# Kernel optimization log

Hardware: AMD Instinct MI355X
Metric: run time of the kernel (lower is better)

Reference implementation:

```python
import jax, jax.numpy as jnp
import numpy as np
from jax import lax

B, T, HID, H, DK, DV, K = 2, 2048, 1024, 16, 64, 64, 4
SCALE = float(DK) ** -0.5
EPS = 1e-5


def setup_inputs() -> dict:
    key = jax.random.key(0)
    ks = jax.random.split(key, 12)
    n = lambda k, sh, s=0.02: (jax.random.normal(k, sh, jnp.float32) * s)
    return {
        "x": jax.random.normal(ks[0], (B, T, HID), jnp.float32),
        "Wq": n(ks[1], (H * DK, HID)),
        "Wk": n(ks[2], (H * DK, HID)),
        "Wv": n(ks[3], (H * DV, HID)),
        "Wa": n(ks[4], (H * DV, HID)), "ba": jnp.zeros((H * DV,), jnp.float32),
        "Wb": n(ks[5], (H, HID)), "bb": jnp.zeros((H,), jnp.float32),
        "Wg": n(ks[6], (H * DV, HID)),
        "Wo": n(ks[7], (HID, H * DV)),
        "qcw": n(ks[8], (H * DK, 1, K), 0.3), "qcb": jnp.zeros((H * DK,), jnp.float32),
        "kcw": n(ks[9], (H * DK, 1, K), 0.3), "kcb": jnp.zeros((H * DK,), jnp.float32),
        "vcw": n(ks[10], (H * DV, 1, K), 0.3), "vcb": jnp.zeros((H * DV,), jnp.float32),
        "ln_w": jnp.ones((DV,), jnp.float32), "ln_b": jnp.zeros((DV,), jnp.float32),
    }


def _causal_dwconv_silu(z, w, b):
    # z: [B,T,C], w: [C,1,K] depthwise. Conv1d(padding=K-1) then slice[:T] == causal left-pad.
    zc = z.transpose(0, 2, 1)  # [B,C,T]
    y = lax.conv_general_dilated(zc, w, (1,), [(K - 1, 0)],
                                 dimension_numbers=("NCH", "OIH", "NCH"),
                                 feature_group_count=zc.shape[1])
    return jax.nn.silu((y + b[None, :, None]).transpose(0, 2, 1))


def reference(x, Wq, Wk, Wv, Wa, ba, Wb, bb, Wg, Wo,
              qcw, qcb, kcw, kcb, vcw, vcb, ln_w, ln_b):
    Bb, Tt, _ = x.shape
    q = _causal_dwconv_silu(x @ Wq.T, qcw, qcb).reshape(Bb, Tt, H, DK)
    k = _causal_dwconv_silu(x @ Wk.T, kcw, kcb).reshape(Bb, Tt, H, DK) * SCALE
    v = _causal_dwconv_silu(x @ Wv.T, vcw, vcb).reshape(Bb, Tt, H, DV)
    a = jax.nn.sigmoid(x @ Wa.T + ba).reshape(Bb, Tt, H, DV)
    beta = jax.nn.sigmoid(x @ Wb.T + bb)  # [B,T,H]

    def step(S, inp):
        qt, kt, vt, at, bt = inp  # qt/kt: [B,H,DK], vt/at: [B,H,DV], bt: [B,H]
        err = jnp.einsum("bhij,bhj->bhi", S, kt) - vt          # S@k - v
        S = at[..., None] * S - bt[..., None, None] * (err[..., None] * kt[:, :, None, :])
        o = jnp.einsum("bhij,bhj->bhi", S, qt)                 # S@q
        return S, o

    xs = tuple(jnp.moveaxis(t, 1, 0) for t in (q, k, v, a, beta))  # time-leading
    S0 = jnp.zeros((Bb, H, DV, DK), x.dtype)
    _, o = lax.scan(step, S0, xs)
    o = jnp.moveaxis(o, 0, 1)  # [B,T,H,DV]

    mu = o.mean(-1, keepdims=True)
    var = ((o - mu) ** 2).mean(-1, keepdims=True)
    o = (o - mu) / jnp.sqrt(var + EPS) * ln_w + ln_b

    g = jax.nn.sigmoid(x @ Wg.T).reshape(Bb, Tt, H, DV)
    o = (o * g).reshape(Bb, Tt, H * DV)
    return o @ Wo.T
```

## Files before the change

kernel.cpp:

```cpp
#include <hip/hip_runtime.h>
#include <hip/hip_bf16.h>
#include <cstdint>


using bf16 = __hip_bfloat16;
typedef __bf16 bf16x8 __attribute__((ext_vector_type(8)));
typedef __bf16 bf16x4v __attribute__((ext_vector_type(4)));
typedef float f32x4 __attribute__((ext_vector_type(4)));
typedef float f32x2 __attribute__((ext_vector_type(2)));
typedef unsigned int u32x4 __attribute__((ext_vector_type(4)));
typedef unsigned int u32x2 __attribute__((ext_vector_type(2)));

__device__ __forceinline__ __bf16 cvt_bf16(float f) {
  __hip_bfloat16 h = (__hip_bfloat16)f;
  return *reinterpret_cast<__bf16*>(&h);
}
__device__ __forceinline__ void async_copy16(const void* g, void* l) {
  __builtin_amdgcn_global_load_lds((const __attribute__((address_space(1))) void*)g,
                                   (__attribute__((address_space(3))) void*)l,
                                   16, 0, 0);
}
__device__ __forceinline__ float bcf(unsigned int u) { return __builtin_bit_cast(float, u); }
template <int CTRL>
__device__ __forceinline__ float dpp_f(float x) {
  int y = __builtin_amdgcn_update_dpp(0, __builtin_bit_cast(int, x), CTRL, 0xF, 0xF, true);
  return __builtin_bit_cast(float, y);
}

__global__ __launch_bounds__(256) void cvtw_kernel(
    const float* __restrict__ x, const float* __restrict__ Wq,
    const float* __restrict__ Wk, const float* __restrict__ Wv,
    const float* __restrict__ Wa, const float* __restrict__ Wg,
    const float* __restrict__ Wo, bf16* __restrict__ xb,
    bf16* __restrict__ w4b, bf16* __restrict__ wgb, bf16* __restrict__ wob)
{
  int blk = blockIdx.x;
  const float* src;
  __bf16* dst;
  size_t off;
  if (blk < 4096) {
    src = x; dst = (__bf16*)xb;
    off = (size_t)blk * 1024 + threadIdx.x * 4;
  } else if (blk < 8192) {
    int wb = blk - 4096;
    int wi = wb >> 10;
    src = (wi == 0) ? Wq : (wi == 1) ? Wk : (wi == 2) ? Wv : Wa;
    dst = (__bf16*)w4b + (size_t)wi * 1024 * 1024;
    off = (size_t)(wb & 1023) * 1024 + threadIdx.x * 4;
  } else if (blk < 9216) {
    src = Wg; dst = (__bf16*)wgb;
    off = (size_t)(blk - 8192) * 1024 + threadIdx.x * 4;
  } else {
    src = Wo; dst = (__bf16*)wob;
    off = (size_t)(blk - 9216) * 1024 + threadIdx.x * 4;
  }
  float4 f = *(const float4*)(src + off);
  bf16x4v t;
  t[0] = cvt_bf16(f.x); t[1] = cvt_bf16(f.y); t[2] = cvt_bf16(f.z); t[3] = cvt_bf16(f.w);
  *(bf16x4v*)(dst + off) = t;
}

template <int MODE, bool A_FP32>
__global__ __launch_bounds__(256) void gemm_bt(
    const void* __restrict__ Av, const float* __restrict__ Bt,
    const float* __restrict__ bias, float* __restrict__ Cf, bf16* __restrict__ Cb,
    int M, int N, int K)
{
  __shared__ __align__(16) __bf16 As[128 * 32];
  __shared__ __align__(16) __bf16 Bs[128 * 32];

  const int tid  = threadIdx.x;
  const int lane = tid & 63;
  const int wave = tid >> 6;
  const int tile_m = blockIdx.y * 128;
  const int tile_n = blockIdx.x * 128;
  const int wm = (wave >> 1) * 64;
  const int wn = (wave & 1) * 64;

  const int srow = lane >> 2;
  const int scol = (lane & 3) * 8;

  f32x4 acc[4][4];
#pragma unroll
  for (int i = 0; i < 4; ++i)
#pragma unroll
    for (int j = 0; j < 4; ++j) acc[i][j] = {0.f, 0.f, 0.f, 0.f};

  for (int k0 = 0; k0 < K; k0 += 32) {
    float4 b0[2], b1[2], a0[2], a1[2];
#pragma unroll
    for (int s = 0; s < 2; ++s) {
      int brow = tile_n + s * 64 + wave * 16 + srow;
      if (brow > N - 1) brow = N - 1;
      const float* bp = Bt + (size_t)brow * K + k0 + scol;
      b0[s] = *(const float4*)bp;
      b1[s] = *(const float4*)(bp + 4);
      if (A_FP32) {
        int arow = tile_m + s * 64 + wave * 16 + srow;
        const float* ap = (const float*)Av + (size_t)arow * K + k0 + scol;
        a0[s] = *(const float4*)ap;
        a1[s] = *(const float4*)(ap + 4);
      }
    }
    __syncthreads();
#pragma unroll
    for (int s = 0; s < 2; ++s) {
      if (!A_FP32) {
        int arow = tile_m + s * 64 + wave * 16 + srow;
        async_copy16((const __bf16*)Av + (size_t)arow * K + k0 + scol,
                     &As[(s * 64 + wave * 16 + srow) * 32 + scol]);
      } else {
        bf16x8 ua;
        ua[0] = cvt_bf16(a0[s].x); ua[1] = cvt_bf16(a0[s].y);
        ua[2] = cvt_bf16(a0[s].z); ua[3] = cvt_bf16(a0[s].w);
        ua[4] = cvt_bf16(a1[s].x); ua[5] = cvt_bf16(a1[s].y);
        ua[6] = cvt_bf16(a1[s].z); ua[7] = cvt_bf16(a1[s].w);
        *(bf16x8*)&As[(s * 64 + wave * 16 + srow) * 32 + scol] = ua;
      }
      bf16x8 u;
      u[0] = cvt_bf16(b0[s].x); u[1] = cvt_bf16(b0[s].y);
      u[2] = cvt_bf16(b0[s].z); u[3] = cvt_bf16(b0[s].w);
      u[4] = cvt_bf16(b1[s].x); u[5] = cvt_bf16(b1[s].y);
      u[6] = cvt_bf16(b1[s].z); u[7] = cvt_bf16(b1[s].w);
      *(bf16x8*)&Bs[(s * 64 + wave * 16 + srow) * 32 + scol] = u;
    }
    __syncthreads();

    bf16x8 af[4], bfr[4];
#pragma unroll
    for (int i = 0; i < 4; ++i)
      af[i] = *(const bf16x8*)&As[(wm + i * 16 + (lane & 15)) * 32 + (lane >> 4) * 8];
#pragma unroll
    for (int j = 0; j < 4; ++j)
      bfr[j] = *(const bf16x8*)&Bs[(wn + j * 16 + (lane & 15)) * 32 + (lane >> 4) * 8];

#pragma unroll
    for (int i = 0; i < 4; ++i)
#pragma unroll
      for (int j = 0; j < 4; ++j)
        acc[i][j] = __builtin_amdgcn_mfma_f32_16x16x32_bf16(af[i], bfr[j], acc[i][j], 0, 0, 0);
  }

#pragma unroll
  for (int i = 0; i < 4; ++i) {
#pragma unroll
    for (int j = 0; j < 4; ++j) {
#pragma unroll
      for (int r = 0; r < 4; ++r) {
        int gm = tile_m + wm + i * 16 + (lane >> 4) * 4 + r;
        int gn = tile_n + wn + j * 16 + (lane & 15);
        if (gn < N) {
          float val = acc[i][j][r];
          if (MODE == 3 || MODE == 5) {
            float bv = bias ? bias[gn] : 0.f;
            val = 1.f / (1.f + __expf(-(val + bv)));
          }
          if (MODE == 4)      Cf[(size_t)gm * N + gn] = val;
          else if (MODE == 5) Cf[(size_t)gn * M + gm] = val;
          else                Cb[(size_t)gm * N + gn] = (bf16)val;
        }
      }
    }
  }
}

__global__ __launch_bounds__(256) void gemm_bb_ln(
    const bf16* __restrict__ o, const bf16* __restrict__ g,
    const float* __restrict__ lnw, const float* __restrict__ lnb,
    const bf16* __restrict__ Bw, float* __restrict__ C)
{
  __shared__ __align__(16) __bf16 As2[64][72];
  __shared__ __align__(16) __bf16 Bs2[2][128][32];
  __shared__ float sW[64], sB[64];

  const int bx = blockIdx.x;
  const int logical = (bx & 7) * 64 + (bx >> 3);
  const int tile_m = (logical >> 3) * 64;
  const int tile_n = (logical & 7) * 128;

  const int tid  = threadIdx.x;
  const int lane = tid & 63;
  const int wave = tid >> 6;
  const int wm = (wave >> 1) * 32;
  const int wn = (wave & 1) * 64;
  const int srow = lane >> 2;
  const int scol = (lane & 3) * 8;
  const int rl  = tid >> 2;
  const int qtr = tid & 3;

  if (tid < 64) { sW[tid] = lnw[tid]; sB[tid] = lnb[tid]; }

  const __bf16* obase = (const __bf16*)o + (size_t)(tile_m + rl) * 1024 + qtr * 16;
  const __bf16* gbase = (const __bf16*)g + (size_t)(tile_m + rl) * 1024 + qtr * 16;

  f32x4 acc[2][4];
#pragma unroll
  for (int i = 0; i < 2; ++i)
#pragma unroll
    for (int j = 0; j < 4; ++j) acc[i][j] = {0.f, 0.f, 0.f, 0.f};

  bf16x8 ov0, ov1, gv0, gv1;
  ov0 = *(const bf16x8*)(obase);
  ov1 = *(const bf16x8*)(obase + 8);
  gv0 = *(const bf16x8*)(gbase);
  gv1 = *(const bf16x8*)(gbase + 8);

  for (int h = 0; h < 16; ++h) {
    bf16x8 no0, no1, ng0, ng1;
    if (h + 1 < 16) {
      const __bf16* op = obase + (h + 1) * 64;
      const __bf16* gp = gbase + (h + 1) * 64;
      no0 = *(const bf16x8*)(op);
      no1 = *(const bf16x8*)(op + 8);
      ng0 = *(const bf16x8*)(gp);
      ng1 = *(const bf16x8*)(gp + 8);
    }

    __syncthreads();

#pragma unroll
    for (int sub = 0; sub < 2; ++sub)
#pragma unroll
      for (int s = 0; s < 2; ++s) {
        int brow = tile_n + s * 64 + wave * 16 + srow;
        async_copy16((const __bf16*)Bw + (size_t)brow * 1024 + h * 64 + sub * 32 + scol,
                     &Bs2[sub][s * 64 + wave * 16 + srow][scol]);
      }

    float sum = 0.f;
#pragma unroll
    for (int e = 0; e < 8; ++e)
      sum += (float)ov0[e] + (float)ov1[e];
    sum += __shfl_xor(sum, 1);
    sum += __shfl_xor(sum, 2);
    float mu = sum * (1.f / 64.f);
    float vv = 0.f;
#pragma unroll
    for (int e = 0; e < 8; ++e) {
      float d0 = (float)ov0[e] - mu, d1 = (float)ov1[e] - mu;
      vv += d0 * d0 + d1 * d1;
    }
    vv += __shfl_xor(vv, 1);
    vv += __shfl_xor(vv, 2);
    float rstd = rsqrtf(vv * (1.f / 64.f) + 1e-5f);

    bf16x8 res0, res1;
#pragma unroll
    for (int e = 0; e < 8; ++e) {
      int c0 = qtr * 16 + e;
      res0[e] = cvt_bf16((((float)ov0[e] - mu) * rstd * sW[c0] + sB[c0]) * (float)gv0[e]);
      res1[e] = cvt_bf16((((float)ov1[e] - mu) * rstd * sW[c0 + 8] + sB[c0 + 8]) * (float)gv1[e]);
    }
    *(bf16x8*)&As2[rl][qtr * 16 + 0] = res0;
    *(bf16x8*)&As2[rl][qtr * 16 + 8] = res1;

    __syncthreads();

#pragma unroll
    for (int sub = 0; sub < 2; ++sub) {
      bf16x8 af[2], bfr[4];
#pragma unroll
      for (int i = 0; i < 2; ++i)
        af[i] = *(const bf16x8*)&As2[wm + i * 16 + (lane & 15)][(lane >> 4) * 8 + sub * 32];
#pragma unroll
      for (int j = 0; j < 4; ++j)
        bfr[j] = *(const bf16x8*)&Bs2[sub][wn + j * 16 + (lane & 15)][(lane >> 4) * 8];

#pragma unroll
      for (int i = 0; i < 2; ++i)
#pragma unroll
        for (int j = 0; j < 4; ++j)
          acc[i][j] = __builtin_amdgcn_mfma_f32_16x16x32_bf16(af[i], bfr[j], acc[i][j], 0, 0, 0);
    }

    if (h + 1 < 16) {
      ov0 = no0; ov1 = no1;
      gv0 = ng0; gv1 = ng1;
    }
  }

#pragma unroll
  for (int i = 0; i < 2; ++i)
#pragma unroll
    for (int j = 0; j < 4; ++j)
#pragma unroll
      for (int r = 0; r < 4; ++r) {
        int gm = tile_m + wm + i * 16 + (lane >> 4) * 4 + r;
        int gn = tile_n + wn + j * 16 + (lane & 15);
        C[(size_t)gm * 1024 + gn] = acc[i][j][r];
      }
}

__global__ __launch_bounds__(256) void mega_gemm2(
    const bf16* __restrict__ Av, const bf16* __restrict__ W4b,
    const float* __restrict__ Wb, const float* __restrict__ bb,
    const float* __restrict__ ba, bf16* __restrict__ C4,
    float* __restrict__ betab)
{
  __shared__ __align__(16) __bf16 As[128 * 32];
  __shared__ __align__(16) __bf16 Bs[128 * 32];

  const int bx = blockIdx.x;
  const bool isbeta = (bx >= 1024);
  int tile_m, tile_n;
  if (!isbeta) {
    const int xcd = bx & 7;
    const int local = bx >> 3;
    const int mg = xcd >> 1;
    const int ng = xcd & 1;
    const int lm = local & 7;
    const int ln = local >> 3;
    tile_m = (mg * 8 + lm) * 128;
    tile_n = (ng * 16 + ln) * 128;
  } else {
    tile_m = (bx - 1024) * 128;
    tile_n = 0;
  }
  const int grp = tile_n >> 10;
  const int tnl = tile_n & 1023;

  const int tid  = threadIdx.x;
  const int lane = tid & 63;
  const int wave = tid >> 6;
  const int wm = (wave >> 1) * 64;
  const int wn = (wave & 1) * 64;

  const int srow = lane >> 2;
  const int scol = (lane & 3) * 8;

  f32x4 acc[4][4];
#pragma unroll
  for (int i = 0; i < 4; ++i)
#pragma unroll
    for (int j = 0; j < 4; ++j) acc[i][j] = {0.f, 0.f, 0.f, 0.f};

  const __bf16* Wp = (const __bf16*)W4b + (size_t)grp * 1024 * 1024;

  for (int k0 = 0; k0 < 1024; k0 += 32) {
    float4 b0[2], b1[2];
    if (isbeta) {
#pragma unroll
      for (int s = 0; s < 2; ++s) {
        int brow = s * 64 + wave * 16 + srow;
        if (brow > 15) brow = 15;
        const float* bp = Wb + (size_t)brow * 1024 + k0 + scol;
        b0[s] = *(const float4*)bp;
        b1[s] = *(const float4*)(bp + 4);
      }
    }
    __syncthreads();
#pragma unroll
    for (int s = 0; s < 2; ++s) {
      int arow = tile_m + s * 64 + wave * 16 + srow;
      async_copy16((const __bf16*)Av + (size_t)arow * 1024 + k0 + scol,
                   &As[(s * 64 + wave * 16 + srow) * 32 + scol]);
      if (!isbeta) {
        int brow = tnl + s * 64 + wave * 16 + srow;
        async_copy16(Wp + (size_t)brow * 1024 + k0 + scol,
                     &Bs[(s * 64 + wave * 16 + srow) * 32 + scol]);
      } else {
        bf16x8 u;
        u[0] = cvt_bf16(b0[s].x); u[1] = cvt_bf16(b0[s].y);
        u[2] = cvt_bf16(b0[s].z); u[3] = cvt_bf16(b0[s].w);
        u[4] = cvt_bf16(b1[s].x); u[5] = cvt_bf16(b1[s].y);
        u[6] = cvt_bf16(b1[s].z); u[7] = cvt_bf16(b1[s].w);
        *(bf16x8*)&Bs[(s * 64 + wave * 16 + srow) * 32 + scol] = u;
      }
    }
    __syncthreads();

    bf16x8 af[4], bfr[4];
#pragma unroll
    for (int i = 0; i < 4; ++i)
      af[i] = *(const bf16x8*)&As[(wm + i * 16 + (lane & 15)) * 32 + (lane >> 4) * 8];
#pragma unroll
    for (int j = 0; j < 4; ++j)
      bfr[j] = *(const bf16x8*)&Bs[(wn + j * 16 + (lane & 15)) * 32 + (lane >> 4) * 8];

#pragma unroll
    for (int i = 0; i < 4; ++i)
#pragma unroll
      for (int j = 0; j < 4; ++j)
        acc[i][j] = __builtin_amdgcn_mfma_f32_16x16x32_bf16(af[i], bfr[j], acc[i][j], 0, 0, 0);
  }

  if (!isbeta) {
    bf16* Cp = (bf16*)((__bf16*)C4 + (size_t)grp * 4096 * 1024);
#pragma unroll
    for (int i = 0; i < 4; ++i)
#pragma unroll
      for (int j = 0; j < 4; ++j)
#pragma unroll
        for (int r = 0; r < 4; ++r) {
          int gm = tile_m + wm + i * 16 + (lane >> 4) * 4 + r;
          int col = tnl + wn + j * 16 + (lane & 15);
          float val = acc[i][j][r];
          if (grp == 3) val = 1.f / (1.f + __expf(-(val + ba[col])));
          ((__bf16*)Cp)[(size_t)gm * 1024 + col] = cvt_bf16(val);
        }
  } else {
#pragma unroll
    for (int i = 0; i < 4; ++i)
#pragma unroll
      for (int j = 0; j < 4; ++j)
#pragma unroll
        for (int r = 0; r < 4; ++r) {
          int gm = tile_m + wm + i * 16 + (lane >> 4) * 4 + r;
          int gn = wn + j * 16 + (lane & 15);
          if (gn < 16) {
            float val = 1.f / (1.f + __expf(-(acc[i][j][r] + bb[gn])));
            betab[(size_t)gn * 4096 + gm] = val;
          }
        }
  }
}

__device__ __forceinline__ void conv_body(
    int idx, const bf16* __restrict__ z, const float* __restrict__ w,
    const float* __restrict__ bias, bf16* __restrict__ out, float scale)
{
  int c8 = idx & 127;
  int m  = idx >> 7;
  int t  = m & 2047;
  int c0 = c8 * 8;

  const __bf16* base = (const __bf16*)z + (size_t)m * 1024 + c0;
  const bf16x8 zzero = __builtin_bit_cast(bf16x8, (u32x4){0u, 0u, 0u, 0u});
  bf16x8 z3 = *(const bf16x8*)base;
  bf16x8 z2 = (t >= 1) ? *(const bf16x8*)(base - 1024) : zzero;
  bf16x8 z1 = (t >= 2) ? *(const bf16x8*)(base - 2048) : zzero;
  bf16x8 z0 = (t >= 3) ? *(const bf16x8*)(base - 3072) : zzero;

  const float* wp = w + c0 * 4;
  bf16x8 res;
#pragma unroll
  for (int e = 0; e < 8; ++e) {
    float4 we = *(const float4*)(wp + e * 4);
    float acc = bias[c0 + e] + (float)z3[e] * we.w;
    acc += (float)z2[e] * we.z;
    acc += (float)z1[e] * we.y;
    acc += (float)z0[e] * we.x;
    float s = acc / (1.f + __expf(-acc));
    res[e] = cvt_bf16(s * scale);
  }
  *(bf16x8*)((__bf16*)out + (size_t)m * 1024 + c0) = res;
}

__global__ __launch_bounds__(256) void conv_silu_kernel(
    const bf16* __restrict__ z, const float* __restrict__ w,
    const float* __restrict__ bias, bf16* __restrict__ out, float scale)
{
  conv_body(blockIdx.x * 256 + threadIdx.x, z, w, bias, out, scale);
}

__global__ __launch_bounds__(256) void conv2_kernel(
    const bf16* __restrict__ zq, const bf16* __restrict__ zk,
    const float* __restrict__ qcw, const float* __restrict__ qcb,
    const float* __restrict__ kcw, const float* __restrict__ kcb,
    bf16* __restrict__ oq, bf16* __restrict__ ok)
{
  int sec = blockIdx.x >> 11;
  int bx  = blockIdx.x & 2047;
  int idx = bx * 256 + threadIdx.x;
  if (sec == 0) conv_body(idx, zq, qcw, qcb, oq, 1.f);
  else          conv_body(idx, zk, kcw, kcb, ok, 0.125f);
}

__global__ __launch_bounds__(256) void convv_kk_kernel(
    const bf16* __restrict__ zv, const float* __restrict__ vcw,
    const float* __restrict__ vcb, bf16* __restrict__ ov,
    const bf16* __restrict__ k, const float* __restrict__ betab,
    float* __restrict__ G)
{
  if (blockIdx.x < 2048) {
    conv_body(blockIdx.x * 256 + threadIdx.x, zv, vcw, vcb, ov, 1.f);
    return;
  }
  int gtid = (blockIdx.x - 2048) * 256 + threadIdx.x;
  int out = gtid >> 2;
  int j   = gtid & 3;
  int h = out >> 12;
  int m = out & 4095;
  int t = m & 2047;
  float s = 0.f;
  if (t > 0) {
    const __bf16* r1 = (const __bf16*)k + (size_t)m * 1024 + h * 64 + j * 16;
    const __bf16* r0 = r1 - 1024;
    bf16x8 a0 = *(const bf16x8*)r0;
    bf16x8 a1 = *(const bf16x8*)(r0 + 8);
    bf16x8 b0 = *(const bf16x8*)r1;
    bf16x8 b1 = *(const bf16x8*)(r1 + 8);
#pragma unroll
    for (int e = 0; e < 8; ++e)
      s += (float)a0[e] * (float)b0[e] + (float)a1[e] * (float)b1[e];
  }
  s += __shfl_xor(s, 1);
  s += __shfl_xor(s, 2);
  if (j == 0) G[out] = betab[out] * s;
}

__global__ __launch_bounds__(256) void kk_kernel(
    const bf16* __restrict__ k, const float* __restrict__ betab,
    float* __restrict__ G)
{
  int tid = blockIdx.x * 256 + threadIdx.x;
  int out = tid >> 2;
  int j   = tid & 3;
  int h = out >> 12;
  int m = out & 4095;
  int t = m & 2047;
  float s = 0.f;
  if (t > 0) {
    const __bf16* r1 = (const __bf16*)k + (size_t)m * 1024 + h * 64 + j * 16;
    const __bf16* r0 = r1 - 1024;
    bf16x8 a0 = *(const bf16x8*)r0;
    bf16x8 a1 = *(const bf16x8*)(r0 + 8);
    bf16x8 b0 = *(const bf16x8*)r1;
    bf16x8 b1 = *(const bf16x8*)(r1 + 8);
#pragma unroll
    for (int e = 0; e < 8; ++e)
      s += (float)a0[e] * (float)b0[e] + (float)a1[e] * (float)b1[e];
  }
  s += __shfl_xor(s, 1);
  s += __shfl_xor(s, 2);
  if (j == 0) G[out] = betab[out] * s;
}

#define SCAN_STEP(i, KN0, KN1, Q0, Q1, WV, WA, BT, GT, LAST)                  \
  {                                                                           \
    const float vr = ((i) & 1) ? bcf((WV) & 0xffff0000u) : bcf((WV) << 16);   \
    const float ar = ((i) & 1) ? bcf((WA) & 0xffff0000u) : bcf((WA) << 16);   \
    float unxt = 0.f;                                                         \
    f32x2 k2n0 = {0.f, 0.f}, k2n1 = {0.f, 0.f};                               \
    if (!(LAST)) {                                                            \
      k2n0 = unpk(KN0); k2n1 = unpk(KN1);                                     \
      f32x2 dd = S20 * k2n0; dd += S21 * k2n1;                                \
      unxt = dd[0] + dd[1];                                                   \
      unxt += dpp_f<0xB1>(unxt);  unxt += dpp_f<0x4E>(unxt);                  \
      unxt += dpp_f<0x141>(unxt); unxt += dpp_f<0x140>(unxt);                 \
    } else { Sold0 = S20; Sold1 = S21; }                                      \
    float A_ = (BT) * __builtin_fmaf(aprev, u, -vr);                          \
    cc = __builtin_fmaf(-cc, (GT), A_);                                       \
    f32x2 q20 = unpk(Q0), q21 = unpk(Q1);                                     \
    const f32x2 cc2 = {cc, cc}, arv = {ar, ar};                               \
    f32x2 oo;                                                                 \
    { f32x2 t0 = cc2 * k2c0; S20 = arv * S20 - t0; oo = S20 * q20;            \
      f32x2 t1 = cc2 * k2c1; S21 = arv * S21 - t1; oo += S21 * q21; }         \
    so[(i)][lane] = oo[0] + oo[1];                                            \
    aprev = ar;                                                               \
    if (!(LAST)) { k2c0 = k2n0; k2c1 = k2n1; u = unxt; }                      \
  }

#define LOADG(KS, QS, VS, AS, BS, GS, g)                                      \
  KS = *(const u32x4*)&skT[buf][sg][(g) * 8];                                 \
  QS = *(const u32x4*)&sqT[buf][sg][(g) * 8];                                 \
  VS = *(const unsigned int*)&svaT[buf][0][r4][(g) * 2];                      \
  AS = *(const unsigned int*)&svaT[buf][1][r4][(g) * 2];                      \
  BS = *(const f32x2*)&sbeta[c * 16 + (g) * 2];                               \
  GS = *(const f32x2*)&sG[c * 16 + (g) * 2];

__global__ __launch_bounds__(256) void scan_gemm_kernel(
    const bf16* __restrict__ q, const bf16* __restrict__ k,
    const bf16* __restrict__ v, const bf16* __restrict__ a,
    const float* __restrict__ betab, const float* __restrict__ gkk,
    bf16* __restrict__ o,
    const float* __restrict__ x, const bf16* __restrict__ Wgb,
    bf16* __restrict__ gout)
{
  __shared__ __align__(16) __bf16 skT[2][16][72];
  __shared__ __align__(16) __bf16 sqT[2][16][72];
  __shared__ __align__(16) __bf16 svaT[2][2][4][16];
  __shared__ __align__(16) float  so[16][68];
  __shared__ __align__(16) __bf16 so2[16][4];
  __shared__ float sbeta[2048];
  __shared__ float sG[2048];
  __shared__ __align__(16) __bf16 As[128 * 32];
  __shared__ __align__(16) __bf16 Bs[128 * 32];

  if (blockIdx.x >= 512) {
    const int gb   = blockIdx.x - 512;
    const int tid  = threadIdx.x;
    const int lane = tid & 63;
    const int wave = tid >> 6;
    const int tile_m = (gb >> 3) * 128;
    const int tile_n = (gb & 7) * 128;
    const int wm = (wave >> 1) * 64;
    const int wn = (wave & 1) * 64;
    const int srow = lane >> 2;
    const int scol = (lane & 3) * 8;

    f32x4 acc[4][4];
#pragma unroll
    for (int i = 0; i < 4; ++i)
#pragma unroll
      for (int j = 0; j < 4; ++j) acc[i][j] = {0.f, 0.f, 0.f, 0.f};

    for (int k0 = 0; k0 < 1024; k0 += 32) {
      float4 a0[2], a1[2];
#pragma unroll
      for (int s = 0; s < 2; ++s) {
        int arow = tile_m + s * 64 + wave * 16 + srow;
        const float* ap = x + (size_t)arow * 1024 + k0 + scol;
        a0[s] = *(const float4*)ap;
        a1[s] = *(const float4*)(ap + 4);
      }
      __syncthreads();
#pragma unroll
      for (int s = 0; s < 2; ++s) {
        bf16x8 ua;
        ua[0] = cvt_bf16(a0[s].x); ua[1] = cvt_bf16(a0[s].y);
        ua[2] = cvt_bf16(a0[s].z); ua[3] = cvt_bf16(a0[s].w);
        ua[4] = cvt_bf16(a1[s].x); ua[5] = cvt_bf16(a1[s].y);
        ua[6] = cvt_bf16(a1[s].z); ua[7] = cvt_bf16(a1[s].w);
        *(bf16x8*)&As[(s * 64 + wave * 16 + srow) * 32 + scol] = ua;
        int brow = tile_n + s * 64 + wave * 16 + srow;
        async_copy16((const __bf16*)Wgb + (size_t)brow * 1024 + k0 + scol,
                     &Bs[(s * 64 + wave * 16 + srow) * 32 + scol]);
      }
      __syncthreads();

      bf16x8 af[4], bfr[4];
#pragma unroll
      for (int i = 0; i < 4; ++i)
        af[i] = *(const bf16x8*)&As[(wm + i * 16 + (lane & 15)) * 32 + (lane >> 4) * 8];
#pragma unroll
      for (int j = 0; j < 4; ++j)
        bfr[j] = *(const bf16x8*)&Bs[(wn + j * 16 + (lane & 15)) * 32 + (lane >> 4) * 8];

#pragma unroll
      for (int i = 0; i < 4; ++i)
#pragma unroll
        for (int j = 0; j < 4; ++j)
          acc[i][j] = __builtin_amdgcn_mfma_f32_16x16x32_bf16(af[i], bfr[j], acc[i][j], 0, 0, 0);
    }

#pragma unroll
    for (int i = 0; i < 4; ++i)
#pragma unroll
      for (int j = 0; j < 4; ++j)
#pragma unroll
        for (int r = 0; r < 4; ++r) {
          int gm = tile_m + wm + i * 16 + (lane >> 4) * 4 + r;
          int gn = tile_n + wn + j * 16 + (lane & 15);
          float val = 1.f / (1.f + __expf(-acc[i][j][r]));
          gout[(size_t)gm * 1024 + gn] = (bf16)val;
        }
    return;
  }

  if (threadIdx.x >= 64) return;
  __builtin_amdgcn_s_setprio(1);

  const int blk = blockIdx.x;
  const int qd = blk >> 5;
  const int bh = blk & 31;
  const int b = bh >> 4, h = bh & 15;
  const int lane = threadIdx.x;
  const int r4 = lane >> 4;
  const int sg = lane & 15;

  {
    const float* bp = betab + (size_t)h * 4096 + b * 2048;
    const float* gp = gkk   + (size_t)h * 4096 + b * 2048;
    for (int t4 = lane * 4; t4 < 2048; t4 += 256) {
      *(float4*)&sbeta[t4] = *(const float4*)(bp + t4);
      *(float4*)&sG[t4]    = *(const float4*)(gp + t4);
    }
  }

  const size_t bkq = (size_t)b * 2048 * 1024 + h * 64;
  const size_t bva = bkq + qd * 4;
  const __bf16* kp = (const __bf16*)k;
  const __bf16* qp = (const __bf16*)q;

  const int g_st = lane >> 3;
  const int g_cg = (lane & 7) * 8;
  const int sgp  = (lane & 7) * 2;
  const int va_vh = (lane >> 4) & 1;
  const int va_st = lane & 15;

  bf16x8 pk0, pk1, pq0, pq1;
  bf16x4v pva;
  auto fetch = [&](int t0) {
    int st0 = t0 + g_st, st1 = t0 + 8 + g_st;
    pk0 = *(const bf16x8*)(kp + bkq + (size_t)st0 * 1024 + g_cg);
    pk1 = *(const bf16x8*)(kp + bkq + (size_t)st1 * 1024 + g_cg);
    pq0 = *(const bf16x8*)(qp + bkq + (size_t)st0 * 1024 + g_cg);
    pq1 = *(const bf16x8*)(qp + bkq + (size_t)st1 * 1024 + g_cg);
    if (lane < 32) {
      const __bf16* src = va_vh ? (const __bf16*)a : (const __bf16*)v;
      pva = *(const bf16x4v*)(src + bva + (size_t)(t0 + va_st) * 1024);
    }
  };
  auto commit = [&](int cb) {
    {
      u32x4 wk = __builtin_bit_cast(u32x4, pk0);
      u32x4 wq = __builtin_bit_cast(u32x4, pq0);
      u32x2 lo, hi;
      lo[0] = wk[0]; lo[1] = wk[1]; hi[0] = wk[2]; hi[1] = wk[3];
      *(u32x2*)&skT[cb][sgp][g_st * 4]     = lo;
      *(u32x2*)&skT[cb][sgp + 1][g_st * 4] = hi;
      lo[0] = wq[0]; lo[1] = wq[1]; hi[0] = wq[2]; hi[1] = wq[3];
      *(u32x2*)&sqT[cb][sgp][g_st * 4]     = lo;
      *(u32x2*)&sqT[cb][sgp + 1][g_st * 4] = hi;
    }
    {
      u32x4 wk = __builtin_bit_cast(u32x4, pk1);
      u32x4 wq = __builtin_bit_cast(u32x4, pq1);
      u32x2 lo, hi;
      lo[0] = wk[0]; lo[1] = wk[1]; hi[0] = wk[2]; hi[1] = wk[3];
      *(u32x2*)&skT[cb][sgp][(8 + g_st) * 4]     = lo;
      *(u32x2*)&skT[cb][sgp + 1][(8 + g_st) * 4] = hi;
      lo[0] = wq[0]; lo[1] = wq[1]; hi[0] = wq[2]; hi[1] = wq[3];
      *(u32x2*)&sqT[cb][sgp][(8 + g_st) * 4]     = lo;
      *(u32x2*)&sqT[cb][sgp + 1][(8 + g_st) * 4] = hi;
    }
    if (lane < 32) {
#pragma unroll
      for (int r = 0; r < 4; ++r) svaT[cb][va_vh][r][va_st] = pva[r];
    }
  };

  fetch(0); commit(0);

  f32x2 S20 = {0.f, 0.f}, S21 = {0.f, 0.f};
  f32x2 Sold0 = {0.f, 0.f}, Sold1 = {0.f, 0.f};
  float u = 0.f, cc = 0.f, aprev = 0.f;

  auto unpk = [&](unsigned int w) -> f32x2 {
    f32x2 r; r[0] = bcf(w << 16); r[1] = bcf(w & 0xffff0000u); return r;
  };

  for (int c = 0; c < 128; ++c) {
    const int buf = c & 1;
    const bool hasNext = (c + 1 < 128);

    if (hasNext) fetch((c + 1) * 16);

    u32x4 kA, qA, kB, qB, kC, qC;
    unsigned int vA, aA, vB, aB, vC, aC;
    f32x2 bA, gA, bB, gB, bC, gC;

    LOADG(kA, qA, vA, aA, bA, gA, 0)
    LOADG(kB, qB, vB, aB, bB, gB, 1)
    LOADG(kC, qC, vC, aC, bC, gC, 2)

    f32x2 k2c0 = unpk(kA[0]);
    f32x2 k2c1 = unpk(kA[1]);
    {
      f32x2 dd = Sold0 * k2c0;
      dd += Sold1 * k2c1;
      float un = dd[0] + dd[1];
      un += dpp_f<0xB1>(un);
      un += dpp_f<0x4E>(un);
      un += dpp_f<0x141>(un);
      un += dpp_f<0x140>(un);
      u = un;
    }

    SCAN_STEP(0,  kA[2], kA[3], qA[0], qA[1], vA, aA, bA[0], gA[0], false)
    SCAN_STEP(1,  kB[0], kB[1], qA[2], qA[3], vA, aA, bA[1], gA[1], false)
    LOADG(kA, qA, vA, aA, bA, gA, 3)
    SCAN_STEP(2,  kB[2], kB[3], qB[0], qB[1], vB, aB, bB[0], gB[0], false)
    SCAN_STEP(3,  kC[0], kC[1], qB[2], qB[3], vB, aB, bB[1], gB[1], false)
    LOADG(kB, qB, vB, aB, bB, gB, 4)
    SCAN_STEP(4,  kC[2], kC[3], qC[0], qC[1], vC, aC, bC[0], gC[0], false)
    SCAN_STEP(5,  kA[0], kA[1], qC[2], qC[3], vC, aC, bC[1], gC[1], false)
    LOADG(kC, qC, vC, aC, bC, gC, 5)
    SCAN_STEP(6,  kA[2], kA[3], qA[0], qA[1], vA, aA, bA[0], gA[0], false)
    SCAN_STEP(7,  kB[0], kB[1], qA[2], qA[3], vA, aA, bA[1], gA[1], false)
    LOADG(kA, qA, vA, aA, bA, gA, 6)
    SCAN_STEP(8,  kB[2], kB[3], qB[0], qB[1], vB, aB, bB[0], gB[0], false)
    SCAN_STEP(9,  kC[0], kC[1], qB[2], qB[3], vB, aB, bB[1], gB[1], false)
    LOADG(kB, qB, vB, aB, bB, gB, 7)
    SCAN_STEP(10, kC[2], kC[3], qC[0], qC[1], vC, aC, bC[0], gC[0], false)
    SCAN_STEP(11, kA[0], kA[1], qC[2], qC[3], vC, aC, bC[1], gC[1], false)
    SCAN_STEP(12, kA[2], kA[3], qA[0], qA[1], vA, aA, bA[0], gA[0], false)
    SCAN_STEP(13, kB[0], kB[1], qA[2], qA[3], vA, aA, bA[1], gA[1], false)
    SCAN_STEP(14, kB[2], kB[3], qB[0], qB[1], vB, aB, bB[0], gB[0], false)
    SCAN_STEP(15, kB[2], kB[3], qB[2], qB[3], vB, aB, bB[1], gB[1], true)

    {
      int st = lane >> 2, rr = lane & 3;
      float4 A0 = *(const float4*)&so[st][rr * 16];
      float4 A1 = *(const float4*)&so[st][rr * 16 + 4];
      float4 A2 = *(const float4*)&so[st][rr * 16 + 8];
      float4 A3 = *(const float4*)&so[st][rr * 16 + 12];
      float s = (((A0.x + A0.y) + (A0.z + A0.w)) + ((A1.x + A1.y) + (A1.z + A1.w)))
              + (((A2.x + A2.y) + (A2.z + A2.w)) + ((A3.x + A3.y) + (A3.z + A3.w)));
      so2[st][rr] = cvt_bf16(s);
    }
    if (lane < 16)
      *(bf16x4v*)((__bf16*)o + bva + (size_t)(c * 16 + lane) * 1024) =
          *(const bf16x4v*)&so2[lane][0];

    if (hasNext) commit(buf ^ 1);
  }
}

__global__ __launch_bounds__(256) void ln_gate_kernel(
    const bf16* __restrict__ o, const bf16* __restrict__ g,
    const float* __restrict__ lnw, const float* __restrict__ lnb,
    bf16* __restrict__ out)
{
  int row = blockIdx.x * 4 + (threadIdx.x >> 6);
  int lane = threadIdx.x & 63;
  size_t idx = (size_t)row * 64 + lane;
  float xv = (float)o[idx];
  float mu = xv;
#pragma unroll
  for (int s = 1; s < 64; s <<= 1) mu += __shfl_xor(mu, s);
  mu *= (1.f / 64.f);
  float d = xv - mu;
  float vv = d * d;
#pragma unroll
  for (int s = 1; s < 64; s <<= 1) vv += __shfl_xor(vv, s);
  vv *= (1.f / 64.f);
  float y = d * rsqrtf(vv + 1e-5f) * lnw[lane] + lnb[lane];
  y *= (float)g[idx];
  out[idx] = (bf16)y;
}

extern "C" void kernel_launch(void* const* d_in, const int* in_sizes, int n_in,
                              void* d_out, int out_size, void* d_ws, size_t ws_size,
                              hipStream_t stream)
{
  const float* x   = (const float*)d_in[0];
  const float* Wq  = (const float*)d_in[1];
  const float* Wk  = (const float*)d_in[2];
  const float* Wv  = (const float*)d_in[3];
  const float* Wa  = (const float*)d_in[4];
  const float* ba  = (const float*)d_in[5];
  const float* Wb  = (const float*)d_in[6];
  const float* bb  = (const float*)d_in[7];
  const float* Wg  = (const float*)d_in[8];
  const float* Wo  = (const float*)d_in[9];
  const float* qcw = (const float*)d_in[10];
  const float* qcb = (const float*)d_in[11];
  const float* kcw = (const float*)d_in[12];
  const float* kcb = (const float*)d_in[13];
  const float* vcw = (const float*)d_in[14];
  const float* vcb = (const float*)d_in[15];
  const float* lnw = (const float*)d_in[16];
  const float* lnb = (const float*)d_in[17];

  const int M = 4096, HID = 1024;
  const size_t PLANE = (size_t)M * HID;
  const size_t PB = PLANE * sizeof(bf16);

  char* ws = (char*)d_ws;
  float* outf = (float*)d_out;
  const bool rich = (ws_size >= 5 * PB + 1024);

  dim3 blk(256);
  dim3 g8(8, 32);
  int nconv = (int)((size_t)M * 128 / 256);

  if (rich) {
    bf16* P0 = (bf16*)(ws);
    bf16* P1 = (bf16*)(ws + PB);
    bf16* P2 = (bf16*)(ws + 2 * PB);
    bf16* P3 = (bf16*)(ws + 3 * PB);
    bf16* P4 = (bf16*)(ws + 4 * PB);
    bf16*  xb    = (bf16*)d_out;
    bf16*  W4b   = (bf16*)((char*)d_out + 8 * 1024 * 1024);
    bf16*  Kb    = xb;
    bf16*  Qb    = W4b;
    float* betab = (float*)P4;
    float* gkk   = (float*)((char*)P4 + 256 * 1024);
    bf16*  Wgb   = (bf16*)((char*)P4 + 1024 * 1024);
    bf16*  Wob   = (bf16*)((char*)P4 + 3 * 1024 * 1024);

    cvtw_kernel<<<10240, blk, 0, stream>>>(x, Wq, Wk, Wv, Wa, Wg, Wo,
                                           xb, W4b, Wgb, Wob);
    mega_gemm2<<<1056, blk, 0, stream>>>(xb, W4b, Wb, bb, ba, P0, betab);
    conv2_kernel<<<4096, blk, 0, stream>>>(P0, P1, qcw, qcb, kcw, kcb, Qb, Kb);
    convv_kk_kernel<<<3072, blk, 0, stream>>>(P2, vcw, vcb, P1, Kb, betab, gkk);
    scan_gemm_kernel<<<768, blk, 0, stream>>>(Qb, Kb, P1, P3, betab, gkk, P0,
                                              x, Wgb, P2);
    gemm_bb_ln<<<512, blk, 0, stream>>>(P0, P2, lnw, lnb, Wob, outf);
  } else {
    bf16* P  = (bf16*)(ws);
    bf16* qb = (bf16*)(ws + PB);
    bf16* kb = (bf16*)(ws + 2 * PB);
    bf16* vb = (bf16*)(ws + 3 * PB);
    float* betab = (float*)d_out;
    float* gkk   = (float*)((char*)d_out + 256 * 1024);
    bf16*  ob    = (bf16*)((char*)d_out + 8 * 1024 * 1024);

    gemm_bt<2, true><<<g8, blk, 0, stream>>>(x, Wq, nullptr, nullptr, P, M, HID, HID);
    conv_silu_kernel<<<nconv, blk, 0, stream>>>(P, qcw, qcb, qb, 1.f);
    gemm_bt<2, true><<<g8, blk, 0, stream>>>(x, Wk, nullptr, nullptr, P, M, HID, HID);
    conv_silu_kernel<<<nconv, blk, 0, stream>>>(P, kcw, kcb, kb, 0.125f);
    gemm_bt<2, true><<<g8, blk, 0, stream>>>(x, Wv, nullptr, nullptr, P, M, HID, HID);
    conv_silu_kernel<<<nconv, blk, 0, stream>>>(P, vcw, vcb, vb, 1.f);
    gemm_bt<3, true><<<g8, blk, 0, stream>>>(x, Wa, ba, nullptr, P, M, HID, HID);
    gemm_bt<5, true><<<dim3(1, 32), blk, 0, stream>>>(x, Wb, bb, betab, nullptr, M, 16, HID);
    kk_kernel<<<1024, blk, 0, stream>>>(kb, betab, gkk);
    scan_gemm_kernel<<<512, blk, 0, stream>>>(qb, kb, vb, P, betab, gkk, ob,
                                              x, nullptr, nullptr);
    gemm_bt<3, true><<<g8, blk, 0, stream>>>(x, Wg, nullptr, nullptr, qb, M, HID, HID);
    ln_gate_kernel<<<M * 16 / 4, blk, 0, stream>>>(ob, qb, lnw, lnb, kb);
    gemm_bt<4, false><<<g8, blk, 0, stream>>>(kb, Wo, nullptr, outf, nullptr, M, HID, HID);
  }
}
```

Baseline: 428.3 us.

## Fuse k·k_prev dot into k-conv kernel and halve output GEMM M-tile

The k causal-conv path now also recomputes the previous timestep's conv output and forms the beta-scaled k_t·k_{t-1} dot product in the same thread group. This removes the separate kk pass that re-read K from memory. The v conv becomes a plain conv launch. The final LN+gate+Wo GEMM drops from 64-row to 32-row tiles, doubling the grid to 1024 blocks for better occupancy, at the cost of less B-tile reuse. The recomputation adds extra exp and FMA work per k element.

```diff
diff --git a/kernel.cpp b/kernel.cpp
--- a/kernel.cpp
+++ b/kernel.cpp
@@ -169,51 +169,43 @@
     const float* __restrict__ lnw, const float* __restrict__ lnb,
     const bf16* __restrict__ Bw, float* __restrict__ C)
 {
-  __shared__ __align__(16) __bf16 As2[64][72];
+  __shared__ __align__(16) __bf16 As2[32][72];
   __shared__ __align__(16) __bf16 Bs2[2][128][32];
   __shared__ float sW[64], sB[64];
 
   const int bx = blockIdx.x;
-  const int logical = (bx & 7) * 64 + (bx >> 3);
-  const int tile_m = (logical >> 3) * 64;
+  const int logical = (bx & 7) * 128 + (bx >> 3);
+  const int tile_m = (logical >> 3) * 32;
   const int tile_n = (logical & 7) * 128;
 
   const int tid  = threadIdx.x;
   const int lane = tid & 63;
   const int wave = tid >> 6;
-  const int wm = (wave >> 1) * 32;
+  const int wm = (wave >> 1) * 16;
   const int wn = (wave & 1) * 64;
   const int srow = lane >> 2;
   const int scol = (lane & 3) * 8;
-  const int rl  = tid >> 2;
-  const int qtr = tid & 3;
+  const int rl  = tid >> 3;
+  const int oct = tid & 7;
 
   if (tid < 64) { sW[tid] = lnw[tid]; sB[tid] = lnb[tid]; }
 
-  const __bf16* obase = (const __bf16*)o + (size_t)(tile_m + rl) * 1024 + qtr * 16;
-  const __bf16* gbase = (const __bf16*)g + (size_t)(tile_m + rl) * 1024 + qtr * 16;
-
-  f32x4 acc[2][4];
-#pragma unroll
-  for (int i = 0; i < 2; ++i)
-#pragma unroll
-    for (int j = 0; j < 4; ++j) acc[i][j] = {0.f, 0.f, 0.f, 0.f};
-
-  bf16x8 ov0, ov1, gv0, gv1;
+  const __bf16* obase = (const __bf16*)o + (size_t)(tile_m + rl) * 1024 + oct * 8;
+  const __bf16* gbase = (const __bf16*)g + (size_t)(tile_m + rl) * 1024 + oct * 8;
+
+  f32x4 acc[1][4];
+#pragma unroll
+  for (int j = 0; j < 4; ++j) acc[0][j] = {0.f, 0.f, 0.f, 0.f};
+
+  bf16x8 ov0, gv0;
   ov0 = *(const bf16x8*)(obase);
-  ov1 = *(const bf16x8*)(obase + 8);
   gv0 = *(const bf16x8*)(gbase);
-  gv1 = *(const bf16x8*)(gbase + 8);
 
   for (int h = 0; h < 16; ++h) {
-    bf16x8 no0, no1, ng0, ng1;
+    bf16x8 no0, ng0;
     if (h + 1 < 16) {
-      const __bf16* op = obase + (h + 1) * 64;
-      const __bf16* gp = gbase + (h + 1) * 64;
-      no0 = *(const bf16x8*)(op);
-      no1 = *(const bf16x8*)(op + 8);
-      ng0 = *(const bf16x8*)(gp);
-      ng1 = *(const bf16x8*)(gp + 8);
+      no0 = *(const bf16x8*)(obase + (h + 1) * 64);
+      ng0 = *(const bf16x8*)(gbase + (h + 1) * 64);
     }
 
     __syncthreads();
@@ -229,66 +221,56 @@
 
     float sum = 0.f;
 #pragma unroll
-    for (int e = 0; e < 8; ++e)
-      sum += (float)ov0[e] + (float)ov1[e];
+    for (int e = 0; e < 8; ++e) sum += (float)ov0[e];
     sum += __shfl_xor(sum, 1);
     sum += __shfl_xor(sum, 2);
+    sum += __shfl_xor(sum, 4);
     float mu = sum * (1.f / 64.f);
     float vv = 0.f;
 #pragma unroll
     for (int e = 0; e < 8; ++e) {
-      float d0 = (float)ov0[e] - mu, d1 = (float)ov1[e] - mu;
-      vv += d0 * d0 + d1 * d1;
+      float d0 = (float)ov0[e] - mu;
+      vv += d0 * d0;
     }
     vv += __shfl_xor(vv, 1);
     vv += __shfl_xor(vv, 2);
+    vv += __shfl_xor(vv, 4);
     float rstd = rsqrtf(vv * (1.f / 64.f) + 1e-5f);
 
-    bf16x8 res0, res1;
+    bf16x8 res0;
 #pragma unroll
     for (int e = 0; e < 8; ++e) {
-      int c0 = qtr * 16 + e;
+      int c0 = oct * 8 + e;
       res0[e] = cvt_bf16((((float)ov0[e] - mu) * rstd * sW[c0] + sB[c0]) * (float)gv0[e]);
-      res1[e] = cvt_bf16((((float)ov1[e] - mu) * rstd * sW[c0 + 8] + sB[c0 + 8]) * (float)gv1[e]);
-    }
-    *(bf16x8*)&As2[rl][qtr * 16 + 0] = res0;
-    *(bf16x8*)&As2[rl][qtr * 16 + 8] = res1;
+    }
+    *(bf16x8*)&As2[rl][oct * 8] = res0;
 
     __syncthreads();
 
 #pragma unroll
     for (int sub = 0; sub < 2; ++sub) {
-      bf16x8 af[2], bfr[4];
-#pragma unroll
-      for (int i = 0; i < 2; ++i)
-        af[i] = *(const bf16x8*)&As2[wm + i * 16 + (lane & 15)][(lane >> 4) * 8 + sub * 32];
+      bf16x8 af, bfr[4];
+      af = *(const bf16x8*)&As2[wm + (lane & 15)][(lane >> 4) * 8 + sub * 32];
 #pragma unroll
       for (int j = 0; j < 4; ++j)
         bfr[j] = *(const bf16x8*)&Bs2[sub][wn + j * 16 + (lane & 15)][(lane >> 4) * 8];
 
 #pragma unroll
-      for (int i = 0; i < 2; ++i)
-#pragma unroll
-        for (int j = 0; j < 4; ++j)
-          acc[i][j] = __builtin_amdgcn_mfma_f32_16x16x32_bf16(af[i], bfr[j], acc[i][j], 0, 0, 0);
-    }
-
-    if (h + 1 < 16) {
-      ov0 = no0; ov1 = no1;
-      gv0 = ng0; gv1 = ng1;
-    }
-  }
-
-#pragma unroll
-  for (int i = 0; i < 2; ++i)
-#pragma unroll
-    for (int j = 0; j < 4; ++j)
-#pragma unroll
-      for (int r = 0; r < 4; ++r) {
-        int gm = tile_m + wm + i * 16 + (lane >> 4) * 4 + r;
-        int gn = tile_n + wn + j * 16 + (lane & 15);
-        C[(size_t)gm * 1024 + gn] = acc[i][j][r];
-      }
+      for (int j = 0; j < 4; ++j)
+        acc[0][j] = __builtin_amdgcn_mfma_f32_16x16x32_bf16(af, bfr[j], acc[0][j], 0, 0, 0);
+    }
+
+    if (h + 1 < 16) { ov0 = no0; gv0 = ng0; }
+  }
+
+#pragma unroll
+  for (int j = 0; j < 4; ++j)
+#pragma unroll
+    for (int r = 0; r < 4; ++r) {
+      int gm = tile_m + wm + (lane >> 4) * 4 + r;
+      int gn = tile_n + wn + j * 16 + (lane & 15);
+      C[(size_t)gm * 1024 + gn] = acc[0][j][r];
+    }
 }
 
 __global__ __launch_bounds__(256) void mega_gemm2(
@@ -457,46 +439,62 @@
     const bf16* __restrict__ zq, const bf16* __restrict__ zk,
     const float* __restrict__ qcw, const float* __restrict__ qcb,
     const float* __restrict__ kcw, const float* __restrict__ kcb,
-    bf16* __restrict__ oq, bf16* __restrict__ ok)
+    bf16* __restrict__ oq, bf16* __restrict__ ok,
+    const float* __restrict__ betab, float* __restrict__ G)
 {
   int sec = blockIdx.x >> 11;
   int bx  = blockIdx.x & 2047;
   int idx = bx * 256 + threadIdx.x;
-  if (sec == 0) conv_body(idx, zq, qcw, qcb, oq, 1.f);
-  else          conv_body(idx, zk, kcw, kcb, ok, 0.125f);
-}
-
-__global__ __launch_bounds__(256) void convv_kk_kernel(
-    const bf16* __restrict__ zv, const float* __restrict__ vcw,
-    const float* __restrict__ vcb, bf16* __restrict__ ov,
-    const bf16* __restrict__ k, const float* __restrict__ betab,
-    float* __restrict__ G)
-{
-  if (blockIdx.x < 2048) {
-    conv_body(blockIdx.x * 256 + threadIdx.x, zv, vcw, vcb, ov, 1.f);
-    return;
-  }
-  int gtid = (blockIdx.x - 2048) * 256 + threadIdx.x;
-  int out = gtid >> 2;
-  int j   = gtid & 3;
-  int h = out >> 12;
-  int m = out & 4095;
-  int t = m & 2047;
-  float s = 0.f;
-  if (t > 0) {
-    const __bf16* r1 = (const __bf16*)k + (size_t)m * 1024 + h * 64 + j * 16;
-    const __bf16* r0 = r1 - 1024;
-    bf16x8 a0 = *(const bf16x8*)r0;
-    bf16x8 a1 = *(const bf16x8*)(r0 + 8);
-    bf16x8 b0 = *(const bf16x8*)r1;
-    bf16x8 b1 = *(const bf16x8*)(r1 + 8);
-#pragma unroll
-    for (int e = 0; e < 8; ++e)
-      s += (float)a0[e] * (float)b0[e] + (float)a1[e] * (float)b1[e];
-  }
-  s += __shfl_xor(s, 1);
-  s += __shfl_xor(s, 2);
-  if (j == 0) G[out] = betab[out] * s;
+  if (sec == 0) { conv_body(idx, zq, qcw, qcb, oq, 1.f); return; }
+
+  int c8 = idx & 127;
+  int m  = idx >> 7;
+  int t  = m & 2047;
+  int c0 = c8 * 8;
+
+  const __bf16* base = (const __bf16*)zk + (size_t)m * 1024 + c0;
+  const bf16x8 zzero = __builtin_bit_cast(bf16x8, (u32x4){0u, 0u, 0u, 0u});
+  bf16x8 z3 = *(const bf16x8*)base;
+  bf16x8 z2 = (t >= 1) ? *(const bf16x8*)(base - 1024) : zzero;
+  bf16x8 z1 = (t >= 2) ? *(const bf16x8*)(base - 2048) : zzero;
+  bf16x8 z0 = (t >= 3) ? *(const bf16x8*)(base - 3072) : zzero;
+  bf16x8 zm4 = (t >= 4) ? *(const bf16x8*)(base - 4096) : zzero;
+
+  const float* wp = kcw + c0 * 4;
+  bf16x8 res;
+  float dot = 0.f;
+#pragma unroll
+  for (int e = 0; e < 8; ++e) {
+    float4 we = *(const float4*)(wp + e * 4);
+    float acc = kcb[c0 + e] + (float)z3[e] * we.w;
+    acc += (float)z2[e] * we.z;
+    acc += (float)z1[e] * we.y;
+    acc += (float)z0[e] * we.x;
+    float s = acc / (1.f + __expf(-acc));
+    res[e] = cvt_bf16(s * 0.125f);
+  }
+  *(bf16x8*)((__bf16*)ok + (size_t)m * 1024 + c0) = res;
+
+  if (t >= 1) {
+#pragma unroll
+    for (int e = 0; e < 8; ++e) {
+      float4 we = *(const float4*)(wp + e * 4);
+      float accp = kcb[c0 + e] + (float)z2[e] * we.w;
+      accp += (float)z1[e] * we.z;
+      accp += (float)z0[e] * we.y;
+      accp += (float)zm4[e] * we.x;
+      float sp = accp / (1.f + __expf(-accp));
+      __bf16 rp = cvt_bf16(sp * 0.125f);
+      dot += (float)rp * (float)res[e];
+    }
+  }
+  dot += __shfl_xor(dot, 1);
+  dot += __shfl_xor(dot, 2);
+  dot += __shfl_xor(dot, 4);
+  if ((threadIdx.x & 7) == 0) {
+    int h = c0 >> 6;
+    G[(size_t)h * 4096 + m] = betab[(size_t)h * 4096 + m] * dot;
+  }
 }
 
 __global__ __launch_bounds__(256) void kk_kernel(
@@ -874,11 +872,12 @@
     cvtw_kernel<<<10240, blk, 0, stream>>>(x, Wq, Wk, Wv, Wa, Wg, Wo,
                                            xb, W4b, Wgb, Wob);
     mega_gemm2<<<1056, blk, 0, stream>>>(xb, W4b, Wb, bb, ba, P0, betab);
-    conv2_kernel<<<4096, blk, 0, stream>>>(P0, P1, qcw, qcb, kcw, kcb, Qb, Kb);
-    convv_kk_kernel<<<3072, blk, 0, stream>>>(P2, vcw, vcb, P1, Kb, betab, gkk);
+    conv2_kernel<<<4096, blk, 0, stream>>>(P0, P1, qcw, qcb, kcw, kcb, Qb, Kb,
+                                           betab, gkk);
+    conv_silu_kernel<<<2048, blk, 0, stream>>>(P2, vcw, vcb, P1, 1.f);
     scan_gemm_kernel<<<768, blk, 0, stream>>>(Qb, Kb, P1, P3, betab, gkk, P0,
                                               x, Wgb, P2);
-    gemm_bb_ln<<<512, blk, 0, stream>>>(P0, P2, lnw, lnb, Wob, outf);
+    gemm_bb_ln<<<1024, blk, 0, stream>>>(P0, P2, lnw, lnb, Wob, outf);
   } else {
     bf16* P  = (bf16*)(ws);
     bf16* qb = (bf16*)(ws + PB);
```

Measured after the change: 441.2 us. 3.0% more time.
